# Performance work log

Hardware: AMD Instinct MI355X
Metric: run time of the kernel (lower is better)

Reference implementation:

```python
import jax, jax.numpy as jnp
import numpy as np

NEG_INF = -jnp.inf


def setup_inputs() -> dict:
    B, T, D = 2, 512, 256
    key = jax.random.key(0)
    ks = jax.random.split(key, 12)
    inp = {
        'x': jax.random.normal(ks[0], (B, T, D), jnp.float32),
        'last_x': jnp.zeros((B, 1, D), jnp.float32),
        'last_num': jnp.zeros((B, 1, D), jnp.float32),
        'last_den': jnp.zeros((B, 1, D), jnp.float32),
        'time_decay': jax.random.normal(ks[1], (D,), jnp.float32) * 0.5,
        'time_first': jax.random.normal(ks[2], (D,), jnp.float32) * 0.5,
        'time_mix_k': jax.random.uniform(ks[3], (1, 1, D), jnp.float32),
        'time_mix_v': jax.random.uniform(ks[4], (1, 1, D), jnp.float32),
        'time_mix_r': jax.random.uniform(ks[5], (1, 1, D), jnp.float32),
        'Wk': jax.random.normal(ks[6], (D, D), jnp.float32) * 0.02,
        'Wv': jax.random.normal(ks[7], (D, D), jnp.float32) * 0.02,
        'Wr': jax.random.normal(ks[8], (D, D), jnp.float32) * 0.02,
        'Wo': jax.random.normal(ks[9], (D, D), jnp.float32) * 0.02,
    }
    return inp


def reference(x, last_x, last_num, last_den, time_decay, time_first,
              time_mix_k, time_mix_v, time_mix_r, Wk, Wv, Wr, Wo):
    B, T, D = x.shape

    # time_shift: prepend last_x, drop last step
    xs = jnp.concatenate([last_x, x[:, :-1, :]], axis=1)  # (B,T,D)

    k = (x * time_mix_k + xs * (1.0 - time_mix_k)) @ Wk.T
    v = (x * time_mix_v + xs * (1.0 - time_mix_v)) @ Wv.T
    r = (x * time_mix_r + xs * (1.0 - time_mix_r)) @ Wr.T
    sr = jax.nn.sigmoid(r)

    # --- run_wkv (quadratic exp-masked formulation, faithful to source) ---
    w = -jnp.exp(time_decay)                      # (D,)
    t = jnp.arange(T + 1, dtype=x.dtype)
    # wt[i, j] = j - i
    wt = t[None, :T] - t[:T, None]                # (T,T)
    tw = w[None, :] * t[1:, None]                 # (T,D): w * (j+1)
    twt = w[None, None, :] * wt[:, :, None]       # (T,T,D)
    # causal mask: -inf where j < i (strictly lower triangle, tril_(-1))
    ii = jnp.arange(T)
    mask = jnp.where(ii[:, None] > ii[None, :], NEG_INF, 0.0).astype(x.dtype)
    ktw = twt[None] + k[:, :, None, :] + mask[None, :, :, None]  # (B,T,T,D)
    etw = jnp.exp(tw)                             # (T,D)
    ektw = jnp.exp(ktw)                           # (B,T,T,D)
    num = etw[None] * last_num + jnp.einsum('bijd,bid->bjd', ektw, v)  # (B,T,D)
    den = etw[None] * last_den + ektw.sum(axis=1)                      # (B,T,D)
    num_prev = jnp.concatenate([last_num, num[:, :-1, :]], axis=1)
    den_prev = jnp.concatenate([last_den, den[:, :-1, :]], axis=1)
    euk = jnp.exp(time_first[None, None, :] + k)
    wkv = (num_prev + euk * v) / (den_prev + euk)
    # ----------------------------------------------------------------------

    out = (wkv * sr) @ Wo.T
    return (out, x[:, -1:, :], num[:, -1:, :], den[:, -1:, :])
```

## Files before the change

### kernel.cpp

```cpp
#include <hip/hip_runtime.h>

#define TT 512
#define DD 256
#define BB 2
#define MM (BB*TT)
#define LCH 16
#define NCH (TT/LCH)

__global__ __launch_bounds__(128)
void gemm_mix_t(const float* __restrict__ X, const float* __restrict__ Xlast,
                const float* __restrict__ W0, const float* __restrict__ W1,
                const float* __restrict__ W2,
                const float* __restrict__ mx0, const float* __restrict__ mx1,
                const float* __restrict__ mx2,
                float* __restrict__ O0, float* __restrict__ O1,
                float* __restrict__ O2)
{
    const int mat = blockIdx.z;
    const float* W  = (mat == 0) ? W0  : (mat == 1) ? W1  : W2;
    const float* mx = (mat == 0) ? mx0 : (mat == 1) ? mx1 : mx2;
    float*       O  = (mat == 0) ? O0  : (mat == 1) ? O1  : O2;

    const int n0  = blockIdx.x * 32;
    const int m0  = blockIdx.y * 64;
    const int b   = m0 / TT;
    const int t0  = m0 % TT;
    const int tid = threadIdx.x;

    const int cc = (tid & 15) * 4;
    const int r8 = tid >> 4;
    const int tm = tid >> 3;
    const int tn = tid & 7;

    __shared__ float As[64][68];
    __shared__ float Bs[64][36];

    float acc[4][4] = {};

    for (int k0 = 0; k0 < DD; k0 += 64) {
        #pragma unroll
        for (int i = 0; i < 8; ++i) {
            const int rr  = r8 + i * 8;
            const int row = m0 + rr;
            const float4 xc = *(const float4*)&X[row * DD + k0 + cc];
            float4 xp;
            if (t0 + rr == 0) xp = *(const float4*)&Xlast[b * DD + k0 + cc];
            else              xp = *(const float4*)&X[(row - 1) * DD + k0 + cc];
            const float4 mv = *(const float4*)&mx[k0 + cc];
            As[cc + 0][rr] = xp.x + (xc.x - xp.x) * mv.x;
            As[cc + 1][rr] = xp.y + (xc.y - xp.y) * mv.y;
            As[cc + 2][rr] = xp.z + (xc.z - xp.z) * mv.z;
            As[cc + 3][rr] = xp.w + (xc.w - xp.w) * mv.w;
        }
        #pragma unroll
        for (int i = 0; i < 4; ++i) {
            const int rr = r8 + i * 8;
            const float4 wv = *(const float4*)&W[(n0 + rr) * DD + k0 + cc];
            Bs[cc + 0][rr] = wv.x;
            Bs[cc + 1][rr] = wv.y;
            Bs[cc + 2][rr] = wv.z;
            Bs[cc + 3][rr] = wv.w;
        }
        __syncthreads();
        #pragma unroll
        for (int kk = 0; kk < 64; ++kk) {
            const float4 a4 = *(const float4*)&As[kk][tm * 4];
            const float4 b4 = *(const float4*)&Bs[kk][tn * 4];
            const float am[4] = {a4.x, a4.y, a4.z, a4.w};
            const float bn[4] = {b4.x, b4.y, b4.z, b4.w};
            #pragma unroll
            for (int i = 0; i < 4; ++i)
                #pragma unroll
                for (int j = 0; j < 4; ++j)
                    acc[i][j] = fmaf(am[i], bn[j], acc[i][j]);
        }
        __syncthreads();
    }

    #pragma unroll
    for (int j = 0; j < 4; ++j) {
        const float4 o = make_float4(acc[0][j], acc[1][j], acc[2][j], acc[3][j]);
        *(float4*)&O[(size_t)(b * DD + n0 + tn * 4 + j) * TT + t0 + tm * 4] = o;
    }
}

__global__ __launch_bounds__(256)
void wkv_scan(const float* __restrict__ kT, const float* __restrict__ vT,
              const float* __restrict__ rT, const float* __restrict__ x,
              const float* __restrict__ last_num, const float* __restrict__ last_den,
              const float* __restrict__ time_decay, const float* __restrict__ time_first,
              float* __restrict__ yT, float* __restrict__ out)
{
    const int tid  = threadIdx.x;
    const int ch   = blockIdx.x * 8 + (tid >> 5);
    const int lane = tid & 31;
    const int b    = ch >> 8;
    const int d    = ch & (DD - 1);

    const float w  = -__expf(time_decay[d]);
    const float ew = __expf(w);
    const float eu = __expf(time_first[d]);

    const size_t base = (size_t)ch * TT + lane * LCH;
    float k_[LCH], v_[LCH], r_[LCH];
    #pragma unroll
    for (int i = 0; i < 4; ++i) {
        *(float4*)&k_[4 * i] = *(const float4*)(kT + base + 4 * i);
        *(float4*)&v_[4 * i] = *(const float4*)(vT + base + 4 * i);
        *(float4*)&r_[4 * i] = *(const float4*)(rT + base + 4 * i);
    }

    float ek[LCH], ekv[LCH], sr[LCH];
    #pragma unroll
    for (int i = 0; i < LCH; ++i) {
        ek[i]  = __expf(k_[i]);
        ekv[i] = ek[i] * v_[i];
        sr[i]  = __builtin_amdgcn_rcpf(1.0f + __expf(-r_[i]));
    }

    float A = __expf(w * (float)LCH);
    float Bn = 0.0f, Bd = 0.0f;
    #pragma unroll
    for (int i = 0; i < LCH; ++i) {
        Bn = fmaf(ew, Bn, ekv[i]);
        Bd = fmaf(ew, Bd, ek[i]);
    }

    #pragma unroll
    for (int s = 1; s < 32; s <<= 1) {
        const float Ax  = __shfl_up(A, s, 32);
        const float Bnx = __shfl_up(Bn, s, 32);
        const float Bdx = __shfl_up(Bd, s, 32);
        if (lane >= s) {
            Bn = fmaf(A, Bnx, Bn);
            Bd = fmaf(A, Bdx, Bd);
            A *= Ax;
        }
    }

    float Aex  = __shfl_up(A, 1, 32);
    float Bnex = __shfl_up(Bn, 1, 32);
    float Bdex = __shfl_up(Bd, 1, 32);
    if (lane == 0) { Aex = 1.0f; Bnex = 0.0f; Bdex = 0.0f; }
    float sn = fmaf(Aex, last_num[ch], Bnex);
    float sd = fmaf(Aex, last_den[ch], Bdex);

    float y_[LCH];
    #pragma unroll
    for (int i = 0; i < LCH; ++i) {
        const float euk = eu * ek[i];
        const float wkv = (sn + eu * ekv[i]) * __builtin_amdgcn_rcpf(sd + euk);
        y_[i] = wkv * sr[i];
        sn = fmaf(ew, sn, ekv[i]);
        sd = fmaf(ew, sd, ek[i]);
    }
    #pragma unroll
    for (int i = 0; i < 4; ++i)
        *(float4*)(yT + base + 4 * i) = *(const float4*)&y_[4 * i];

    if (lane == 31) {
        out[MM * DD + BB * DD + ch]     = sn;
        out[MM * DD + 2 * BB * DD + ch] = sd;
    }
    if (lane == 0)
        out[MM * DD + ch] = x[(b * TT + TT - 1) * DD + d];
}

__global__ __launch_bounds__(64)
void gemm_out(const float* __restrict__ yT, const float* __restrict__ Wo,
              float* __restrict__ O)
{
    const int n0  = blockIdx.x * 32;
    const int m0  = blockIdx.y * 32;
    const int b   = m0 >> 9;
    const int t0  = m0 & (TT - 1);
    const int tid = threadIdx.x;

    __shared__ float As[64][36];
    __shared__ float Bs[64][36];

    const int tm = tid >> 3;
    const int tn = tid & 7;

    float acc[4][4] = {};

    for (int k0 = 0; k0 < DD; k0 += 64) {
        {
            const int mq = (tid & 7) * 4;
            #pragma unroll
            for (int i = 0; i < 8; ++i) {
                const int kk = (tid >> 3) + i * 8;
                *(float4*)&As[kk][mq] =
                    *(const float4*)&yT[(size_t)(b * DD + k0 + kk) * TT + t0 + mq];
            }
        }
        {
            const int cc = (tid & 15) * 4;
            #pragma unroll
            for (int i = 0; i < 8; ++i) {
                const int rr = (tid >> 4) + i * 4;
                const float4 wv = *(const float4*)&Wo[(n0 + rr) * DD + k0 + cc];
                Bs[cc + 0][rr] = wv.x;
                Bs[cc + 1][rr] = wv.y;
                Bs[cc + 2][rr] = wv.z;
                Bs[cc + 3][rr] = wv.w;
            }
        }
        __syncthreads();
        #pragma unroll
        for (int kk = 0; kk < 64; ++kk) {
            const float4 a4 = *(const float4*)&As[kk][tm * 4];
            const float4 b4 = *(const float4*)&Bs[kk][tn * 4];
            const float am[4] = {a4.x, a4.y, a4.z, a4.w};
            const float bn[4] = {b4.x, b4.y, b4.z, b4.w};
            #pragma unroll
            for (int i = 0; i < 4; ++i)
                #pragma unroll
                for (int j = 0; j < 4; ++j)
                    acc[i][j] = fmaf(am[i], bn[j], acc[i][j]);
        }
        __syncthreads();
    }

    #pragma unroll
    for (int i = 0; i < 4; ++i) {
        const float4 o = make_float4(acc[i][0], acc[i][1], acc[i][2], acc[i][3]);
        *(float4*)&O[(size_t)(m0 + tm * 4 + i) * DD + n0 + tn * 4] = o;
    }
}

extern "C" void kernel_launch(void* const* d_in, const int* in_sizes, int n_in,
                              void* d_out, int out_size, void* d_ws, size_t ws_size,
                              hipStream_t stream)
{
    const float* x    = (const float*)d_in[0];
    const float* lx   = (const float*)d_in[1];
    const float* lnum = (const float*)d_in[2];
    const float* lden = (const float*)d_in[3];
    const float* td   = (const float*)d_in[4];
    const float* tf   = (const float*)d_in[5];
    const float* mk   = (const float*)d_in[6];
    const float* mv   = (const float*)d_in[7];
    const float* mr   = (const float*)d_in[8];
    const float* Wk   = (const float*)d_in[9];
    const float* Wv   = (const float*)d_in[10];
    const float* Wr   = (const float*)d_in[11];
    const float* Wo   = (const float*)d_in[12];
    float* out = (float*)d_out;

    float* kT = (float*)d_ws;
    float* vT = kT + MM * DD;
    float* rT = vT + MM * DD;
    float* yT = rT + MM * DD;

    gemm_mix_t<<<dim3(8, 16, 3), 128, 0, stream>>>(
        x, lx, Wk, Wv, Wr, mk, mv, mr, kT, vT, rT);

    wkv_scan<<<dim3(64), 256, 0, stream>>>(
        kT, vT, rT, x, lnum, lden, td, tf, yT, out);

    gemm_out<<<dim3(8, 32), 64, 0, stream>>>(yT, Wo, out);
}
```

Before: 111.7 us.

## Retile both GEMMs to 32x32 tiles with 256 threads and register double-buffering

Both projection GEMMs move to 32x32 output tiles computed by 256 threads, each producing 4 outputs instead of 16. Global loads for the next K-chunk are prefetched into registers while the current chunk is computed from shared memory. The input GEMM now stores tiles in row-major shared layout with float4 stores instead of scalar transposed stores. This doubles the block count of the first GEMM and quadruples threads per block in the output GEMM to raise occupancy and hide latency. The cost is lower per-thread register reuse, so each FMA needs more shared-memory reads.

```diff
diff --git a/kernel.cpp b/kernel.cpp
--- a/kernel.cpp
+++ b/kernel.cpp
@@ -5,9 +5,8 @@
 #define BB 2
 #define MM (BB*TT)
 #define LCH 16
-#define NCH (TT/LCH)
-
-__global__ __launch_bounds__(128)
+
+__global__ __launch_bounds__(256)
 void gemm_mix_t(const float* __restrict__ X, const float* __restrict__ Xlast,
                 const float* __restrict__ W0, const float* __restrict__ W1,
                 const float* __restrict__ W2,
@@ -22,66 +21,69 @@
     float*       O  = (mat == 0) ? O0  : (mat == 1) ? O1  : O2;
 
     const int n0  = blockIdx.x * 32;
-    const int m0  = blockIdx.y * 64;
-    const int b   = m0 / TT;
-    const int t0  = m0 % TT;
+    const int m0  = blockIdx.y * 32;
+    const int b   = m0 >> 9;
+    const int t0  = m0 & (TT - 1);
     const int tid = threadIdx.x;
 
-    const int cc = (tid & 15) * 4;
-    const int r8 = tid >> 4;
-    const int tm = tid >> 3;
-    const int tn = tid & 7;
-
-    __shared__ float As[64][68];
-    __shared__ float Bs[64][36];
-
-    float acc[4][4] = {};
-
-    for (int k0 = 0; k0 < DD; k0 += 64) {
-        #pragma unroll
-        for (int i = 0; i < 8; ++i) {
-            const int rr  = r8 + i * 8;
-            const int row = m0 + rr;
-            const float4 xc = *(const float4*)&X[row * DD + k0 + cc];
+    const int tm = tid >> 5;
+    const int tn = tid & 31;
+
+    __shared__ float As[32][68];
+    __shared__ float Bs[32][68];
+
+    const int rowS[2] = { tid >> 4, (tid + 256) >> 4 };
+    const int c4S[2]  = { (tid & 15) * 4, (tid & 15) * 4 };
+
+    float4 aR[2][2], wR[2][2];
+
+    auto load_chunk = [&](int k0, float4 aO[2], float4 wO[2]) {
+        #pragma unroll
+        for (int p = 0; p < 2; ++p) {
+            const int row = rowS[p], c4 = c4S[p];
+            const float4 xc = *(const float4*)&X[(m0 + row) * DD + k0 + c4];
             float4 xp;
-            if (t0 + rr == 0) xp = *(const float4*)&Xlast[b * DD + k0 + cc];
-            else              xp = *(const float4*)&X[(row - 1) * DD + k0 + cc];
-            const float4 mv = *(const float4*)&mx[k0 + cc];
-            As[cc + 0][rr] = xp.x + (xc.x - xp.x) * mv.x;
-            As[cc + 1][rr] = xp.y + (xc.y - xp.y) * mv.y;
-            As[cc + 2][rr] = xp.z + (xc.z - xp.z) * mv.z;
-            As[cc + 3][rr] = xp.w + (xc.w - xp.w) * mv.w;
-        }
-        #pragma unroll
-        for (int i = 0; i < 4; ++i) {
-            const int rr = r8 + i * 8;
-            const float4 wv = *(const float4*)&W[(n0 + rr) * DD + k0 + cc];
-            Bs[cc + 0][rr] = wv.x;
-            Bs[cc + 1][rr] = wv.y;
-            Bs[cc + 2][rr] = wv.z;
-            Bs[cc + 3][rr] = wv.w;
-        }
-        __syncthreads();
-        #pragma unroll
-        for (int kk = 0; kk < 64; ++kk) {
-            const float4 a4 = *(const float4*)&As[kk][tm * 4];
-            const float4 b4 = *(const float4*)&Bs[kk][tn * 4];
-            const float am[4] = {a4.x, a4.y, a4.z, a4.w};
-            const float bn[4] = {b4.x, b4.y, b4.z, b4.w};
+            if (t0 + row == 0) xp = *(const float4*)&Xlast[b * DD + k0 + c4];
+            else               xp = *(const float4*)&X[(m0 + row - 1) * DD + k0 + c4];
+            const float4 mv = *(const float4*)&mx[k0 + c4];
+            aO[p].x = xp.x + (xc.x - xp.x) * mv.x;
+            aO[p].y = xp.y + (xc.y - xp.y) * mv.y;
+            aO[p].z = xp.z + (xc.z - xp.z) * mv.z;
+            aO[p].w = xp.w + (xc.w - xp.w) * mv.w;
+            wO[p] = *(const float4*)&W[(n0 + row) * DD + k0 + c4];
+        }
+    };
+
+    float acc[4] = {0.f, 0.f, 0.f, 0.f};
+
+    load_chunk(0, aR[0], wR[0]);
+
+    for (int c = 0; c < 4; ++c) {
+        const int cur = c & 1;
+        #pragma unroll
+        for (int p = 0; p < 2; ++p) {
+            *(float4*)&As[rowS[p]][c4S[p]] = aR[cur][p];
+            *(float4*)&Bs[rowS[p]][c4S[p]] = wR[cur][p];
+        }
+        __syncthreads();
+        if (c < 3) load_chunk(64 * (c + 1), aR[cur ^ 1], wR[cur ^ 1]);
+        #pragma unroll
+        for (int k4 = 0; k4 < 16; ++k4) {
+            const float4 bq = *(const float4*)&Bs[tn][k4 * 4];
             #pragma unroll
-            for (int i = 0; i < 4; ++i)
-                #pragma unroll
-                for (int j = 0; j < 4; ++j)
-                    acc[i][j] = fmaf(am[i], bn[j], acc[i][j]);
-        }
-        __syncthreads();
-    }
-
-    #pragma unroll
-    for (int j = 0; j < 4; ++j) {
-        const float4 o = make_float4(acc[0][j], acc[1][j], acc[2][j], acc[3][j]);
-        *(float4*)&O[(size_t)(b * DD + n0 + tn * 4 + j) * TT + t0 + tm * 4] = o;
-    }
+            for (int i = 0; i < 4; ++i) {
+                const float4 aq = *(const float4*)&As[tm * 4 + i][k4 * 4];
+                acc[i] = fmaf(aq.x, bq.x, acc[i]);
+                acc[i] = fmaf(aq.y, bq.y, acc[i]);
+                acc[i] = fmaf(aq.z, bq.z, acc[i]);
+                acc[i] = fmaf(aq.w, bq.w, acc[i]);
+            }
+        }
+        __syncthreads();
+    }
+
+    *(float4*)&O[(size_t)(b * DD + n0 + tn) * TT + t0 + tm * 4] =
+        make_float4(acc[0], acc[1], acc[2], acc[3]);
 }
 
 __global__ __launch_bounds__(256)
@@ -166,7 +168,7 @@
         out[MM * DD + ch] = x[(b * TT + TT - 1) * DD + d];
 }
 
-__global__ __launch_bounds__(64)
+__global__ __launch_bounds__(256)
 void gemm_out(const float* __restrict__ yT, const float* __restrict__ Wo,
               float* __restrict__ O)
 {
@@ -176,57 +178,59 @@
     const int t0  = m0 & (TT - 1);
     const int tid = threadIdx.x;
 
+    const int tm = tid >> 5;
+    const int tn = tid & 31;
+
     __shared__ float As[64][36];
-    __shared__ float Bs[64][36];
-
-    const int tm = tid >> 3;
-    const int tn = tid & 7;
-
-    float acc[4][4] = {};
-
-    for (int k0 = 0; k0 < DD; k0 += 64) {
-        {
-            const int mq = (tid & 7) * 4;
+    __shared__ float Bs[32][68];
+
+    const int rowA[2] = { tid >> 3, (tid + 256) >> 3 };
+    const int c4A     = (tid & 7) * 4;
+    const int rowB[2] = { tid >> 4, (tid + 256) >> 4 };
+    const int c4B     = (tid & 15) * 4;
+
+    float4 aR[2][2], wR[2][2];
+
+    auto load_chunk = [&](int k0, float4 aO[2], float4 wO[2]) {
+        #pragma unroll
+        for (int p = 0; p < 2; ++p) {
+            aO[p] = *(const float4*)&yT[(size_t)(b * DD + k0 + rowA[p]) * TT + t0 + c4A];
+            wO[p] = *(const float4*)&Wo[(n0 + rowB[p]) * DD + k0 + c4B];
+        }
+    };
+
+    float acc[4] = {0.f, 0.f, 0.f, 0.f};
+
+    load_chunk(0, aR[0], wR[0]);
+
+    for (int c = 0; c < 4; ++c) {
+        const int cur = c & 1;
+        #pragma unroll
+        for (int p = 0; p < 2; ++p) {
+            *(float4*)&As[rowA[p]][c4A] = aR[cur][p];
+            *(float4*)&Bs[rowB[p]][c4B] = wR[cur][p];
+        }
+        __syncthreads();
+        if (c < 3) load_chunk(64 * (c + 1), aR[cur ^ 1], wR[cur ^ 1]);
+        #pragma unroll
+        for (int k4 = 0; k4 < 16; ++k4) {
+            const float4 bq = *(const float4*)&Bs[tn][k4 * 4];
+            const float bb[4] = {bq.x, bq.y, bq.z, bq.w};
             #pragma unroll
-            for (int i = 0; i < 8; ++i) {
-                const int kk = (tid >> 3) + i * 8;
-                *(float4*)&As[kk][mq] =
-                    *(const float4*)&yT[(size_t)(b * DD + k0 + kk) * TT + t0 + mq];
+            for (int j = 0; j < 4; ++j) {
+                const float4 aq = *(const float4*)&As[k4 * 4 + j][tm * 4];
+                acc[0] = fmaf(aq.x, bb[j], acc[0]);
+                acc[1] = fmaf(aq.y, bb[j], acc[1]);
+                acc[2] = fmaf(aq.z, bb[j], acc[2]);
+                acc[3] = fmaf(aq.w, bb[j], acc[3]);
             }
         }
-        {
-            const int cc = (tid & 15) * 4;
-            #pragma unroll
-            for (int i = 0; i < 8; ++i) {
-                const int rr = (tid >> 4) + i * 4;
-                const float4 wv = *(const float4*)&Wo[(n0 + rr) * DD + k0 + cc];
-                Bs[cc + 0][rr] = wv.x;
-                Bs[cc + 1][rr] = wv.y;
-                Bs[cc + 2][rr] = wv.z;
-                Bs[cc + 3][rr] = wv.w;
-            }
-        }
-        __syncthreads();
-        #pragma unroll
-        for (int kk = 0; kk < 64; ++kk) {
-            const float4 a4 = *(const float4*)&As[kk][tm * 4];
-            const float4 b4 = *(const float4*)&Bs[kk][tn * 4];
-            const float am[4] = {a4.x, a4.y, a4.z, a4.w};
-            const float bn[4] = {b4.x, b4.y, b4.z, b4.w};
-            #pragma unroll
-            for (int i = 0; i < 4; ++i)
-                #pragma unroll
-                for (int j = 0; j < 4; ++j)
-                    acc[i][j] = fmaf(am[i], bn[j], acc[i][j]);
-        }
-        __syncthreads();
-    }
-
-    #pragma unroll
-    for (int i = 0; i < 4; ++i) {
-        const float4 o = make_float4(acc[i][0], acc[i][1], acc[i][2], acc[i][3]);
-        *(float4*)&O[(size_t)(m0 + tm * 4 + i) * DD + n0 + tn * 4] = o;
-    }
+        __syncthreads();
+    }
+
+    #pragma unroll
+    for (int i = 0; i < 4; ++i)
+        O[(size_t)(m0 + tm * 4 + i) * DD + n0 + tn] = acc[i];
 }
 
 extern "C" void kernel_launch(void* const* d_in, const int* in_sizes, int n_in,
@@ -253,11 +257,11 @@
     float* rT = vT + MM * DD;
     float* yT = rT + MM * DD;
 
-    gemm_mix_t<<<dim3(8, 16, 3), 128, 0, stream>>>(
+    gemm_mix_t<<<dim3(8, 32, 3), 256, 0, stream>>>(
         x, lx, Wk, Wv, Wr, mk, mv, mr, kT, vT, rT);
 
     wkv_scan<<<dim3(64), 256, 0, stream>>>(
         kT, vT, rT, x, lnum, lden, td, tf, yT, out);
 
-    gemm_out<<<dim3(8, 32), 64, 0, stream>>>(yT, Wo, out);
-}
+    gemm_out<<<dim3(8, 32), 256, 0, stream>>>(yT, Wo, out);
+}
```

Result: no change. 113.6 us (+1.7%).
